# Performance work log

Hardware: AMD Instinct MI355X
Metric: run time of the kernel (lower is better)

Reference implementation:

```python
import jax, jax.numpy as jnp
import numpy as np

N_BLOCKS = 96
N = N_BLOCKS ** 2          # number of image blocks = n_blocks^2
D = 1024                   # feature dim (fixed by Linear(1024+1, 128))
EPS_COS = 1e-6             # eps of F.cosine_similarity
EPS_BN = 1e-5              # BatchNorm1d eps


def setup_inputs() -> dict:
    key = jax.random.key(0)
    ks = jax.random.split(key, 6)
    return {
        "features": jax.random.normal(ks[0], (N, D), dtype=jnp.float32),
        "scores": jax.random.uniform(ks[1], (N,), dtype=jnp.float32),
        "W1": jax.random.normal(ks[2], (D + 1, 128), dtype=jnp.float32) * 0.03,
        "b1": jnp.zeros((128,), jnp.float32),
        "g1": jnp.ones((128,), jnp.float32),
        "be1": jnp.zeros((128,), jnp.float32),
        "W2": jax.random.normal(ks[3], (128, 64), dtype=jnp.float32) * 0.08,
        "b2": jnp.zeros((64,), jnp.float32),
        "g2": jnp.ones((64,), jnp.float32),
        "be2": jnp.zeros((64,), jnp.float32),
        "W3": jax.random.normal(ks[4], (64, 1), dtype=jnp.float32) * 0.12,
        "b3": jnp.zeros((1,), jnp.float32),
    }


def _gaussian_similarity(features):
    # Vectorized form of the O(N^2) pairwise loop:
    #   cos_ij = <f_i, f_j> / max(|f_i||f_j|, eps)
    #   sigma^2 = D * (0.5 + 0.5 * cos)  ->  2*sigma^2 = D * (1 + cos)
    #   sim_ij = exp(-|f_i - f_j|^2 / (2*sigma^2)),  sim_ii = 1
    sq = jnp.sum(features * features, axis=-1)          # [N] squared norms
    gram = features @ features.T                          # [N, N] big GEMM
    norms = jnp.sqrt(sq)
    cos = gram / jnp.maximum(norms[:, None] * norms[None, :], EPS_COS)
    d2 = jnp.maximum(sq[:, None] + sq[None, :] - 2.0 * gram, 0.0)
    denom = jnp.maximum(jnp.float32(D) * (1.0 + cos), EPS_COS)
    sim = jnp.exp(-d2 / denom)
    eye = jnp.eye(sim.shape[0], dtype=bool)
    return jnp.where(eye, jnp.float32(1.0), sim)


def _bn_eval(h, gamma, beta):
    # BatchNorm1d in eval mode with init running stats (mean=0, var=1).
    return gamma * (h / jnp.sqrt(1.0 + EPS_BN)) + beta


def reference(features, scores, W1, b1, g1, be1, W2, b2, g2, be2, W3, b3):
    sim = _gaussian_similarity(features)                  # [N, N]
    x = jnp.concatenate([features, scores[:, None]], axis=1)  # [N, D+1]
    h = jax.nn.relu(_bn_eval(x @ W1 + b1, g1, be1))       # [N, 128]
    h = jax.nn.relu(_bn_eval(h @ W2 + b2, g2, be2))       # [N, 64]
    agg = jax.nn.sigmoid(h @ W3 + b3)[:, 0]               # [N]
    sim_mean = jnp.mean(sim, axis=1)                      # [N]
    # Torch broadcast [N,1] * [N] -> [N,N], then .mean() == mean(agg)*mean(sim_mean)
    return jnp.mean(agg) * jnp.mean(sim_mean)


if __name__ == "__main__":
    out = reference(**setup_inputs())
    print(out)
```

## Files before the change

kernel.cpp:

```cpp
#include <hip/hip_runtime.h>

#define N_IMG 9216
#define DFEAT 1024
#define NBP 36
#define NPAIR2 666

typedef __attribute__((ext_vector_type(8))) short short8;
typedef __attribute__((ext_vector_type(4))) float floatx4;
typedef __attribute__((ext_vector_type(16))) float floatx16;
typedef __attribute__((ext_vector_type(4))) int intx4;
typedef __attribute__((ext_vector_type(8))) int intx8;

#define C1F 0.0014088818759657845f
#define C2F 0.05308355472172724f

__device__ __forceinline__ void async_copy16(const void* g, void* l) {
  __builtin_amdgcn_global_load_lds((const __attribute__((address_space(1))) void*)g,
                                   (__attribute__((address_space(3))) void*)l,
                                   16, 0, 0);
}

__device__ __forceinline__ unsigned short f2bf(float x) {
  union { float f; unsigned u; } a; a.f = x;
  unsigned u = a.u;
  u += 0x7fffu + ((u >> 16) & 1u);
  return (unsigned short)(u >> 16);
}

__device__ __forceinline__ unsigned q4(float z) {
  unsigned sg = (__float_as_uint(z) >> 28) & 8u;
  float a = fabsf(z);
  unsigned c = (a < 0.25f) ? 0u : (a < 0.75f) ? 1u : (a < 1.25f) ? 2u :
               (a < 1.75f) ? 3u : (a < 2.5f)  ? 4u : (a < 3.5f)  ? 5u :
               (a < 5.0f)  ? 6u : 7u;
  return c | sg;
}
__device__ __forceinline__ unsigned short pk4(float4 v, float sc) {
  unsigned b0 = q4(v.x * sc) | (q4(v.y * sc) << 4);
  unsigned b1 = q4(v.z * sc) | (q4(v.w * sc) << 4);
  return (unsigned short)(b0 | (b1 << 8));
}

__global__ __launch_bounds__(256) void convert_prep(const float* __restrict__ f,
                                                    const float* __restrict__ W1,
                                                    unsigned char* __restrict__ fbT,
                                                    float* __restrict__ sL,
                                                    float* __restrict__ pL,
                                                    unsigned short* __restrict__ W1t,
                                                    double* __restrict__ sums,
                                                    unsigned* __restrict__ ctr) {
  int b = blockIdx.x, t = threadIdx.x;
  if (b < 2304) {
    int lane = t & 63, wave = t >> 6;
    int row = b * 4 + wave;
    const float4* src = (const float4*)f + (size_t)row * 256;
    float4 v0 = src[lane], v1 = src[64 + lane], v2 = src[128 + lane], v3 = src[192 + lane];
    float s = v0.x * v0.x + v0.y * v0.y + v0.z * v0.z + v0.w * v0.w
            + v1.x * v1.x + v1.y * v1.y + v1.z * v1.z + v1.w * v1.w
            + v2.x * v2.x + v2.y * v2.y + v2.z * v2.z + v2.w * v2.w
            + v3.x * v3.x + v3.y * v3.y + v3.z * v3.z + v3.w * v3.w;
#pragma unroll
    for (int off = 32; off > 0; off >>= 1) s += __shfl_xor(s, off, 64);
    float zsc = rsqrtf(s) * 32.f;
    unsigned short u0 = pk4(v0, zsc), u1 = pk4(v1, zsc),
                   u2 = pk4(v2, zsc), u3 = pk4(v3, zsc);
    unsigned e = lane & 15;
    unsigned sw = (row >> 2) & 1;
    unsigned char* tb = fbT + (size_t)(row >> 5) * 16384 + (row & 31) * 32
                      + (((e >> 3) ^ sw) * 16) + (e & 7) * 2;
    int ko = (lane >> 4) * 1024;
    *(unsigned short*)(tb + ko) = u0;
    *(unsigned short*)(tb + ko + 4096) = u1;
    *(unsigned short*)(tb + ko + 8192) = u2;
    *(unsigned short*)(tb + ko + 12288) = u3;
    if (lane == 0) {
      sL[row] = s * C1F;
      pL[row] = sqrtf(s) * C2F;
    }
  } else {
    int j = b - 2304;
    if (j == 0) {
      if (t < 2) sums[t] = 0.0;
      if (t == 2) *ctr = 0u;
    }
    for (int k = t; k < DFEAT; k += 256)
      W1t[(size_t)j * DFEAT + k] = f2bf(W1[(size_t)k * 128 + j]);
  }
}

__global__ __launch_bounds__(512, 2) void gram_sim(const unsigned char* __restrict__ fbT,
                                                   const float* __restrict__ sL,
                                                   const float* __restrict__ pL,
                                                   double* __restrict__ sums) {
  __shared__ __align__(16) unsigned char stg[2][16384];
  __shared__ float sA[256], pA[256], sB[256], pB[256];
  __shared__ float wpart[8];

  int bid = blockIdx.x, t = threadIdx.x, lane = t & 63, wave = t >> 6;
  int xcd = bid & 7, t8 = bid >> 3;
  int L = (xcd < 2 ? xcd * 84 : 168 + (xcd - 2) * 83) + t8;
  int rem = L, bcol = 0;
  while (rem > bcol) { rem -= (bcol + 1); bcol++; }
  int brow = rem;

  if (t < 256) { sA[t] = sL[brow * 256 + t]; pA[t] = pL[brow * 256 + t]; }
  else { int u = t & 255; sB[u] = sL[bcol * 256 + u]; pB[u] = pL[bcol * 256 + u]; }

  const int spanel = (wave < 4) ? brow : bcol;
  const int slab0 = (wave < 4) ? (2 * wave) : (2 * wave - 8);
  const unsigned char* src0 = fbT + (size_t)(spanel * 8 + slab0) * 16384 + lane * 16;
  const unsigned char* src1 = src0 + 16384;
  char* dst0 = (char*)stg + wave * 2048 + lane * 16;

#define STAGE(buf, kb)                                              \
  {                                                                 \
    async_copy16(src0 + (kb) * 1024, dst0 + (buf) * 16384);         \
    async_copy16(src1 + (kb) * 1024, dst0 + 1024 + (buf) * 16384);  \
  }

  const int r32 = lane & 31, kh = lane >> 5;
  const int swz = (r32 >> 2) & 1;
  const int loff = r32 * 32 + ((kh ^ swz) << 4);
  const int wr = (wave & 1) * 128, wc = (wave >> 1) * 64;
  const char* aBase = (const char*)stg + ((wave & 1) * 4) * 1024 + loff;
  const char* bBase = (const char*)stg + 8192 + ((wave >> 1) * 2) * 1024 + loff;

  floatx16 acc[4][2];
#pragma unroll
  for (int mi = 0; mi < 4; mi++)
#pragma unroll
    for (int ni = 0; ni < 2; ni++)
#pragma unroll
      for (int e = 0; e < 16; e++) acc[mi][ni][e] = 0.f;

  intx8 A8[4], B8[2];
#pragma unroll
  for (int mi = 0; mi < 4; mi++)
#pragma unroll
    for (int e = 0; e < 8; e++) A8[mi][e] = 0;
#pragma unroll
  for (int ni = 0; ni < 2; ni++)
#pragma unroll
    for (int e = 0; e < 8; e++) B8[ni][e] = 0;

  STAGE(0, 0)
  STAGE(1, 1)
#pragma unroll
  for (int kb = 0; kb < 16; kb++) {
    if (kb < 15) asm volatile("s_waitcnt vmcnt(2)" ::: "memory");
    else         asm volatile("s_waitcnt vmcnt(0)" ::: "memory");
    __builtin_amdgcn_s_barrier();
    __builtin_amdgcn_sched_barrier(0);
    const int cur = (kb & 1) * 16384;
#pragma unroll
    for (int mi = 0; mi < 4; mi++) {
      intx4 v = *(const intx4*)(aBase + cur + mi * 1024);
      A8[mi][0] = v[0]; A8[mi][1] = v[1]; A8[mi][2] = v[2]; A8[mi][3] = v[3];
    }
#pragma unroll
    for (int ni = 0; ni < 2; ni++) {
      intx4 v = *(const intx4*)(bBase + cur + ni * 1024);
      B8[ni][0] = v[0]; B8[ni][1] = v[1]; B8[ni][2] = v[2]; B8[ni][3] = v[3];
    }
#pragma unroll
    for (int mi = 0; mi < 4; mi++)
#pragma unroll
      for (int ni = 0; ni < 2; ni++)
        acc[mi][ni] = __builtin_amdgcn_mfma_scale_f32_32x32x64_f8f6f4(
            A8[mi], B8[ni], acc[mi][ni], 4, 4,
            0, 0x7F7F7F7F, 0, 0x7F7F7F7F);
    __builtin_amdgcn_s_barrier();
    __builtin_amdgcn_sched_barrier(0);
    if (kb < 14) STAGE((kb & 1), kb + 2)
  }
#undef STAGE

  const bool diag = (brow == bcol);
  float lsum = 0.f;
#pragma unroll
  for (int ni = 0; ni < 2; ni++) {
    int j_loc = wc + ni * 32 + r32;
    float sj = sB[j_loc], pj = pB[j_loc];
#pragma unroll
    for (int mi = 0; mi < 4; mi++) {
      int rbase = wr + mi * 32 + 4 * kh;
#pragma unroll
      for (int reg = 0; reg < 16; reg++) {
        int i_loc = rbase + (reg & 3) + 8 * (reg >> 2);
        float g = acc[mi][ni][reg];
        float si = sA[i_loc], pi = pA[i_loc];
        float r = __builtin_amdgcn_rcpf(1024.f + g);
        float del = pi * pj;
        float gam = si + sj + del;
        float sim = __builtin_amdgcn_exp2f(fmaf(-1024.f, gam * r, del));
        if (!diag) {
          lsum += sim;
        } else {
          lsum += (i_loc < j_loc) ? 2.f * sim : (i_loc == j_loc ? 1.f : 0.f);
        }
      }
    }
  }
  if (!diag) lsum *= 2.f;
#pragma unroll
  for (int off = 32; off > 0; off >>= 1) lsum += __shfl_down(lsum, off, 64);
  if (lane == 0) wpart[wave] = lsum;
  __syncthreads();
  if (t == 0) {
    float bs = 0.f;
#pragma unroll
    for (int w = 0; w < 8; w++) bs += wpart[w];
    atomicAdd(&sums[0], (double)bs);
  }
}

__global__ __launch_bounds__(256) void mlp_full(const float* __restrict__ f,
                                                const unsigned short* __restrict__ W1t,
                                                const float* __restrict__ scores,
                                                const float* __restrict__ W1,
                                                const float* __restrict__ b1,
                                                const float* __restrict__ g1,
                                                const float* __restrict__ be1,
                                                const float* __restrict__ W2, const float* __restrict__ b2,
                                                const float* __restrict__ g2, const float* __restrict__ be2,
                                                const float* __restrict__ W3, const float* __restrict__ b3,
                                                double* __restrict__ sums,
                                                unsigned* __restrict__ ctr,
                                                float* __restrict__ out) {
  int r0 = blockIdx.x * 32;

  __shared__ __align__(16) float As32[32 * 64];
  __shared__ __align__(16) unsigned short Bs[128 * 64];
  __shared__ float h1s[32][128];
  __shared__ float h2s[32][65];
  __shared__ float sc[32], b1s[128], g1s[128], be1s[128], wls[128], ls[32];

  int t = threadIdx.x, lane = t & 63, wave = t >> 6;
  if (t < 32) sc[t] = scores[r0 + t];
  if (t < 128) {
    b1s[t] = b1[t]; g1s[t] = g1[t]; be1s[t] = be1[t];
    wls[t] = W1[(size_t)DFEAT * 128 + t];
  }

  floatx4 acc[4];
#pragma unroll
  for (int b = 0; b < 4; b++) acc[b] = (floatx4){0.f, 0.f, 0.f, 0.f};

  const int wr = (wave & 1) * 16, wc = (wave >> 1) * 64;

  for (int k0 = 0; k0 < DFEAT; k0 += 64) {
    __syncthreads();
    {
      int c = t, rA = c >> 4, p = c & 15, l = p ^ (rA & 15);
      async_copy16(f + (size_t)(r0 + rA) * DFEAT + k0 + l * 4, (char*)As32 + c * 16);
      c = t + 256; rA = c >> 4; p = c & 15; l = p ^ (rA & 15);
      async_copy16(f + (size_t)(r0 + rA) * DFEAT + k0 + l * 4, (char*)As32 + c * 16);
#pragma unroll
      for (int q = 0; q < 4; q++) {
        int cc = t + q * 256, rB = cc >> 3, pp = cc & 7, ll = pp ^ (rB & 7);
        async_copy16(W1t + (size_t)rB * DFEAT + k0 + ll * 8, (char*)Bs + cc * 16);
      }
    }
    __syncthreads();

    const int mrow = lane & 15;
#pragma unroll
    for (int ks = 0; ks < 2; ks++) {
      const int kq = ks * 32 + (lane >> 4) * 8;
      short8 a, b[4];
      {
        int row = wr + mrow;
        int l0 = kq >> 2;
        int p0 = l0 ^ (row & 15), p1 = (l0 + 1) ^ (row & 15);
        float4 f0 = *(const float4*)&As32[row * 64 + p0 * 4];
        float4 f1 = *(const float4*)&As32[row * 64 + p1 * 4];
        a[0] = (short)f2bf(f0.x); a[1] = (short)f2bf(f0.y);
        a[2] = (short)f2bf(f0.z); a[3] = (short)f2bf(f0.w);
        a[4] = (short)f2bf(f1.x); a[5] = (short)f2bf(f1.y);
        a[6] = (short)f2bf(f1.z); a[7] = (short)f2bf(f1.w);
      }
#pragma unroll
      for (int nt = 0; nt < 4; nt++) {
        int row = wc + nt * 16 + mrow;
        int p = (kq >> 3) ^ (row & 7);
        b[nt] = *(const short8*)&Bs[row * 64 + p * 8];
      }
#pragma unroll
      for (int nt = 0; nt < 4; nt++)
        acc[nt] = __builtin_amdgcn_mfma_f32_16x16x32_bf16(a, b[nt], acc[nt], 0, 0, 0);
    }
  }

  const float inv = 1.0f / sqrtf(1.0f + 1e-5f);
  const int rq = (lane >> 4) * 4, cn = lane & 15;
#pragma unroll
  for (int nt = 0; nt < 4; nt++) {
    int j = wc + nt * 16 + cn;
    float bj = b1s[j], gj = g1s[j] * inv, bej = be1s[j], wj = wls[j];
#pragma unroll
    for (int rr = 0; rr < 4; rr++) {
      int iL = wr + rq + rr;
      float pre = acc[nt][rr] + sc[iL] * wj + bj;
      h1s[iL][j] = fmaxf(gj * pre + bej, 0.f);
    }
  }
  __syncthreads();

  {
    int j = t & 63, rg = (t >> 6) * 8;
    float a2[8];
#pragma unroll
    for (int rr = 0; rr < 8; rr++) a2[rr] = 0.f;
    for (int k = 0; k < 128; k++) {
      float w = W2[k * 64 + j];
#pragma unroll
      for (int rr = 0; rr < 8; rr++) a2[rr] = fmaf(h1s[rg + rr][k], w, a2[rr]);
    }
    float scv = g2[j] * inv, bi = b2[j], be = be2[j];
#pragma unroll
    for (int rr = 0; rr < 8; rr++)
      h2s[rg + rr][j] = fmaxf(scv * (a2[rr] + bi) + be, 0.f);
  }
  __syncthreads();

  if (t < 32) {
    float z = b3[0];
#pragma unroll
    for (int k = 0; k < 64; k++) z = fmaf(h2s[t][k], W3[k], z);
    ls[t] = 1.f / (1.f + __expf(-z));
  }
  __syncthreads();
  if (t == 0) {
    float s = 0.f;
#pragma unroll
    for (int iL = 0; iL < 32; iL++) s += ls[iL];
    atomicAdd(&sums[1], (double)s);
    __threadfence();
    unsigned prev = atomicAdd(ctr, 1u);
    if (prev == 287u) {
      __threadfence();
      double s0 = ((volatile double*)sums)[0];
      double s1 = ((volatile double*)sums)[1];
      out[0] = (float)((s1 / (double)N_IMG) * (s0 / ((double)N_IMG * (double)N_IMG)));
    }
  }
}

extern "C" void kernel_launch(void* const* d_in, const int* in_sizes, int n_in,
                              void* d_out, int out_size, void* d_ws, size_t ws_size,
                              hipStream_t stream) {
  const float* f      = (const float*)d_in[0];
  const float* scores = (const float*)d_in[1];
  const float* W1 = (const float*)d_in[2];
  const float* b1 = (const float*)d_in[3];
  const float* g1 = (const float*)d_in[4];
  const float* be1 = (const float*)d_in[5];
  const float* W2 = (const float*)d_in[6];
  const float* b2 = (const float*)d_in[7];
  const float* g2 = (const float*)d_in[8];
  const float* be2 = (const float*)d_in[9];
  const float* W3 = (const float*)d_in[10];
  const float* b3 = (const float*)d_in[11];

  char* ws = (char*)d_ws;
  unsigned char* fbT  = (unsigned char*)ws;
  float* sL           = (float*)(ws + 4718592);
  float* pL           = (float*)(ws + 4755456);
  unsigned short* W1t = (unsigned short*)(ws + 4792320);
  double* sums        = (double*)(ws + 5054464);
  unsigned* ctr       = (unsigned*)(ws + 5054480);

  convert_prep<<<2432, 256, 0, stream>>>(f, W1, fbT, sL, pL, W1t, sums, ctr);
  gram_sim<<<NPAIR2, 512, 0, stream>>>(fbT, sL, pL, sums);
  mlp_full<<<288, 256, 0, stream>>>(f, W1t, scores, W1, b1, g1, be1,
                                    W2, b2, g2, be2, W3, b3, sums, ctr,
                                    (float*)d_out);
}
```

Baseline: 193.6 us.

## Stage four K-chunks per barrier in gram GEMM and drop LDS swizzle

The gram GEMM's LDS staging now copies four 1 KB K-chunks per stage for both panels into a much larger double buffer (2×64 KB). It then runs four inner MFMA sub-steps between barriers, so the loop has four iterations instead of sixteen. The intent is to cut barrier and wait overhead and let more loads be in flight per synchronisation. The XOR swizzle is removed from both the pack kernel and the LDS read offsets. That risks LDS bank conflicts. The 128 KB+ per-block LDS footprint also likely caps residency at one block per CU despite launch_bounds(512,2).

```diff
diff --git a/kernel.cpp b/kernel.cpp
--- a/kernel.cpp
+++ b/kernel.cpp
@@ -64,10 +64,7 @@
     float zsc = rsqrtf(s) * 32.f;
     unsigned short u0 = pk4(v0, zsc), u1 = pk4(v1, zsc),
                    u2 = pk4(v2, zsc), u3 = pk4(v3, zsc);
-    unsigned e = lane & 15;
-    unsigned sw = (row >> 2) & 1;
-    unsigned char* tb = fbT + (size_t)(row >> 5) * 16384 + (row & 31) * 32
-                      + (((e >> 3) ^ sw) * 16) + (e & 7) * 2;
+    unsigned char* tb = fbT + (size_t)(row >> 5) * 16384 + (row & 31) * 32 + (lane & 15) * 2;
     int ko = (lane >> 4) * 1024;
     *(unsigned short*)(tb + ko) = u0;
     *(unsigned short*)(tb + ko + 4096) = u1;
@@ -92,7 +89,7 @@
                                                    const float* __restrict__ sL,
                                                    const float* __restrict__ pL,
                                                    double* __restrict__ sums) {
-  __shared__ __align__(16) unsigned char stg[2][16384];
+  __shared__ __align__(16) unsigned char stg[2][65536];
   __shared__ float sA[256], pA[256], sB[256], pB[256];
   __shared__ float wpart[8];
 
@@ -105,25 +102,31 @@
 
   if (t < 256) { sA[t] = sL[brow * 256 + t]; pA[t] = pL[brow * 256 + t]; }
   else { int u = t & 255; sB[u] = sL[bcol * 256 + u]; pB[u] = pL[bcol * 256 + u]; }
-
-  const int spanel = (wave < 4) ? brow : bcol;
-  const int slab0 = (wave < 4) ? (2 * wave) : (2 * wave - 8);
-  const unsigned char* src0 = fbT + (size_t)(spanel * 8 + slab0) * 16384 + lane * 16;
-  const unsigned char* src1 = src0 + 16384;
-  char* dst0 = (char*)stg + wave * 2048 + lane * 16;
-
-#define STAGE(buf, kb)                                              \
-  {                                                                 \
-    async_copy16(src0 + (kb) * 1024, dst0 + (buf) * 16384);         \
-    async_copy16(src1 + (kb) * 1024, dst0 + 1024 + (buf) * 16384);  \
+  __syncthreads();
+
+  const unsigned char* srcA = fbT + (size_t)(brow * 8 + wave) * 16384 + lane * 16;
+  const unsigned char* srcB = fbT + (size_t)(bcol * 8 + wave) * 16384 + lane * 16;
+  char* dstA = (char*)stg + wave * 4096 + lane * 16;
+  char* dstB = (char*)stg + 32768 + wave * 4096 + lane * 16;
+
+#define STAGE(buf, q)                                                     \
+  {                                                                       \
+    const int go = (q) * 4096, lo = (buf) * 65536;                        \
+    async_copy16(srcA + go,        dstA + lo);                            \
+    async_copy16(srcA + go + 1024, dstA + lo + 1024);                     \
+    async_copy16(srcA + go + 2048, dstA + lo + 2048);                     \
+    async_copy16(srcA + go + 3072, dstA + lo + 3072);                     \
+    async_copy16(srcB + go,        dstB + lo);                            \
+    async_copy16(srcB + go + 1024, dstB + lo + 1024);                     \
+    async_copy16(srcB + go + 2048, dstB + lo + 2048);                     \
+    async_copy16(srcB + go + 3072, dstB + lo + 3072);                     \
   }
 
   const int r32 = lane & 31, kh = lane >> 5;
-  const int swz = (r32 >> 2) & 1;
-  const int loff = r32 * 32 + ((kh ^ swz) << 4);
+  const int loff = r32 * 32 + kh * 16;
   const int wr = (wave & 1) * 128, wc = (wave >> 1) * 64;
-  const char* aBase = (const char*)stg + ((wave & 1) * 4) * 1024 + loff;
-  const char* bBase = (const char*)stg + 8192 + ((wave >> 1) * 2) * 1024 + loff;
+  const char* aBase = (const char*)stg + ((wave & 1) * 4) * 4096 + loff;
+  const char* bBase = (const char*)stg + 32768 + ((wave >> 1) * 2) * 4096 + loff;
 
   floatx16 acc[4][2];
 #pragma unroll
@@ -133,45 +136,43 @@
 #pragma unroll
       for (int e = 0; e < 16; e++) acc[mi][ni][e] = 0.f;
 
-  intx8 A8[4], B8[2];
-#pragma unroll
-  for (int mi = 0; mi < 4; mi++)
-#pragma unroll
-    for (int e = 0; e < 8; e++) A8[mi][e] = 0;
-#pragma unroll
-  for (int ni = 0; ni < 2; ni++)
-#pragma unroll
-    for (int e = 0; e < 8; e++) B8[ni][e] = 0;
+  union u8x { intx8 v8; intx4 q[2]; };
+  u8x A8[4], B8[2];
+#pragma unroll
+  for (int mi = 0; mi < 4; mi++) A8[mi].q[1] = (intx4){0, 0, 0, 0};
+#pragma unroll
+  for (int ni = 0; ni < 2; ni++) B8[ni].q[1] = (intx4){0, 0, 0, 0};
 
   STAGE(0, 0)
   STAGE(1, 1)
 #pragma unroll
-  for (int kb = 0; kb < 16; kb++) {
-    if (kb < 15) asm volatile("s_waitcnt vmcnt(2)" ::: "memory");
-    else         asm volatile("s_waitcnt vmcnt(0)" ::: "memory");
+  for (int q = 0; q < 4; q++) {
+    if (q < 3) asm volatile("s_waitcnt vmcnt(8)" ::: "memory");
+    else       asm volatile("s_waitcnt vmcnt(0)" ::: "memory");
     __builtin_amdgcn_s_barrier();
     __builtin_amdgcn_sched_barrier(0);
-    const int cur = (kb & 1) * 16384;
-#pragma unroll
-    for (int mi = 0; mi < 4; mi++) {
-      intx4 v = *(const intx4*)(aBase + cur + mi * 1024);
-      A8[mi][0] = v[0]; A8[mi][1] = v[1]; A8[mi][2] = v[2]; A8[mi][3] = v[3];
-    }
-#pragma unroll
-    for (int ni = 0; ni < 2; ni++) {
-      intx4 v = *(const intx4*)(bBase + cur + ni * 1024);
-      B8[ni][0] = v[0]; B8[ni][1] = v[1]; B8[ni][2] = v[2]; B8[ni][3] = v[3];
-    }
-#pragma unroll
-    for (int mi = 0; mi < 4; mi++)
+    const int cur = (q & 1) * 65536;
+#pragma unroll
+    for (int c = 0; c < 4; c++) {
+      const int co = cur + c * 1024;
+#pragma unroll
+      for (int mi = 0; mi < 4; mi++)
+        A8[mi].q[0] = *(const intx4*)(aBase + co + mi * 4096);
 #pragma unroll
       for (int ni = 0; ni < 2; ni++)
-        acc[mi][ni] = __builtin_amdgcn_mfma_scale_f32_32x32x64_f8f6f4(
-            A8[mi], B8[ni], acc[mi][ni], 4, 4,
-            0, 0x7F7F7F7F, 0, 0x7F7F7F7F);
+        B8[ni].q[0] = *(const intx4*)(bBase + co + ni * 4096);
+#pragma unroll
+      for (int mi = 0; mi < 4; mi++)
+#pragma unroll
+        for (int ni = 0; ni < 2; ni++)
+          acc[mi][ni] = __builtin_amdgcn_mfma_scale_f32_32x32x64_f8f6f4(
+              A8[mi].v8, B8[ni].v8, acc[mi][ni], 4, 4,
+              0, 0x7F7F7F7F, 0, 0x7F7F7F7F);
+    }
+    __builtin_amdgcn_sched_barrier(0);
     __builtin_amdgcn_s_barrier();
     __builtin_amdgcn_sched_barrier(0);
-    if (kb < 14) STAGE((kb & 1), kb + 2)
+    if (q < 2) STAGE((q & 1), q + 2)
   }
 #undef STAGE
 
```

Result: faster. 187.3 us (-3.2%).
